# Kernel optimization log

Measured on AMD Instinct MI355X. Metric: run time of the kernel, lower is better.

## Reference

```python
import jax, jax.numpy as jnp
import numpy as np

NUM_ENT = 40000
NUM_REL = 100
EMBED_DIM = 256
FEAT_DIM = 768
BATCH = 32
SEQ_LEN = 3
MASK_POS = 2
EPS = 1e-12


def setup_inputs() -> dict:
    key = jax.random.key(0)
    k1, k2, k3, k4 = jax.random.split(key, 4)
    ent_pkl = jax.random.normal(k1, (NUM_ENT, FEAT_DIM), dtype=jnp.float32)
    other_emb = jax.random.normal(k2, (NUM_ENT + NUM_REL + 3 - NUM_ENT, EMBED_DIM), dtype=jnp.float32)
    proj_W = jax.random.normal(k3, (EMBED_DIM, FEAT_DIM), dtype=jnp.float32) * (1.0 / np.sqrt(FEAT_DIM))
    batch_input_ids = jax.random.randint(k4, (BATCH, SEQ_LEN), 0, NUM_ENT + NUM_REL + 3, dtype=jnp.int64)
    return {
        "ent_pkl": ent_pkl,
        "other_emb": other_emb,
        "proj_W": proj_W,
        "batch_input_ids": batch_input_ids,
        "batch_mask_position": MASK_POS,
    }


def reference(ent_pkl, other_emb, proj_W, batch_input_ids, batch_mask_position):
    # unity embeddings: [other[0], proj(ent_pkl), other[1:]] -> [num_ent+num_rel+3, d]
    ent_proj = ent_pkl @ proj_W.T  # Linear(feat_dim, embed_dim, bias=False)
    unity = jnp.concatenate([other_emb[:1], ent_proj, other_emb[1:]], axis=0)

    mp = int(batch_mask_position)
    # drop the masked slot, keep up to 3 tokens total -> [B, 2]
    query_input = jnp.concatenate(
        [batch_input_ids[:, :mp], batch_input_ids[:, mp + 1:3]], axis=1)
    query_emb = unity[query_input]  # [B, 2, d]
    # F.normalize(dim=-1): x / max(||x||_2, eps)
    norm = jnp.sqrt(jnp.sum(query_emb * query_emb, axis=-1, keepdims=True))
    query_emb = query_emb / jnp.maximum(norm, EPS)
    query_sum = jnp.sum(query_emb, axis=1)  # [B, d]

    E_embed = unity[:NUM_ENT + 1]  # [num_ent+1, d]
    # broadcast L1 distance: [B, num_ent+1]
    score = -jnp.sum(jnp.abs(query_sum[:, None, :] - E_embed[None, :, :]), axis=-1)
    return score
```

## Files before the change

### kernel.cpp

```cpp
#include <hip/hip_runtime.h>
#include <hip/hip_bf16.h>
#include <stdint.h>

#define NE 40000
#define FD 768
#define ED 256
#define NB 32
#define OUTC (NE + 1)

typedef __bf16 bf16x8 __attribute__((ext_vector_type(8)));
typedef float f32x4 __attribute__((ext_vector_type(4)));
typedef unsigned short ushortx8 __attribute__((ext_vector_type(8)));

#define WS_QS 0
#define WS_N01 (32 * 1024)
#define WS_WB (96 * 1024)

__device__ __forceinline__ unsigned short f2bf(float x) {
    union { float f; unsigned u; } v; v.f = x;
    unsigned r = v.u + 0x7fffu + ((v.u >> 16) & 1u);
    return (unsigned short)(r >> 16);
}

__global__ __launch_bounds__(256) void prep_kernel(
    const float* __restrict__ ent_pkl, const float* __restrict__ W,
    const int* __restrict__ ids, const int* __restrict__ mpos,
    unsigned short* __restrict__ Wb, float* __restrict__ n01_raw)
{
    const int bid = blockIdx.x;
    const int t = threadIdx.x;

    if (bid < 192) {
        int i = bid * 1024 + t * 4;
        float4 v = *(const float4*)(W + i);
        ushort4 o;
        o.x = f2bf(v.x); o.y = f2bf(v.y); o.z = f2bf(v.z); o.w = f2bf(v.w);
        *(ushort4*)(Wb + i) = o;
        return;
    }

    __shared__ float row[FD];
    const int slot = bid - 192;
    const int b = slot >> 1, s = slot & 1;
    const int mp = mpos[0];
    const int col = (s < mp) ? s : s + 1;
    const bool wide = (ids[1] == 0 && ids[3] == 0 && ids[5] == 0);
    const int flat = b * 3 + col;
    const int idx = wide ? ids[flat * 2] : ids[flat];
    if (!(idx >= 1 && idx <= NE)) return;

    const float* src = ent_pkl + (size_t)(idx - 1) * FD;
    for (int k = t; k < FD; k += 256) row[k] = src[k];
    __syncthreads();

    const float4* w4 = (const float4*)(W + (size_t)t * FD);
    const float4* r4 = (const float4*)row;
    float a0 = 0.f, a1 = 0.f, a2 = 0.f, a3 = 0.f;
#pragma unroll 2
    for (int k4 = 0; k4 < FD / 4; k4 += 4) {
        float4 w0 = w4[k4 + 0], r0 = r4[k4 + 0];
        float4 w1 = w4[k4 + 1], r1 = r4[k4 + 1];
        float4 w2 = w4[k4 + 2], r2 = r4[k4 + 2];
        float4 w3 = w4[k4 + 3], r3 = r4[k4 + 3];
        a0 += w0.x * r0.x + w0.y * r0.y + w0.z * r0.z + w0.w * r0.w;
        a1 += w1.x * r1.x + w1.y * r1.y + w1.z * r1.z + w1.w * r1.w;
        a2 += w2.x * r2.x + w2.y * r2.y + w2.z * r2.z + w2.w * r2.w;
        a3 += w3.x * r3.x + w3.y * r3.y + w3.z * r3.z + w3.w * r3.w;
    }
    n01_raw[slot * ED + t] = (a0 + a1) + (a2 + a3);
}

__global__ __launch_bounds__(256) void qsum_kernel(
    const float* __restrict__ other_emb, const float* __restrict__ n01_raw,
    const int* __restrict__ ids, const int* __restrict__ mpos,
    float* __restrict__ qs, float* __restrict__ out)
{
    __shared__ float red[4];
    __shared__ float nshare;
    const int b = blockIdx.x, t = threadIdx.x;
    const int mp = mpos[0];
    const bool wide = (ids[1] == 0 && ids[3] == 0 && ids[5] == 0);

    float q = 0.f;
#pragma unroll
    for (int s = 0; s < 2; ++s) {
        const int col = (s < mp) ? s : s + 1;
        const int flat = b * 3 + col;
        const int idx = wide ? ids[flat * 2] : ids[flat];
        float v;
        if (idx >= 1 && idx <= NE) v = n01_raw[(b * 2 + s) * ED + t];
        else if (idx == 0) v = other_emb[t];
        else v = other_emb[(size_t)(idx - NE) * ED + t];

        float ss = v * v;
#pragma unroll
        for (int o = 32; o > 0; o >>= 1) ss += __shfl_down(ss, o, 64);
        if ((t & 63) == 0) red[t >> 6] = ss;
        __syncthreads();
        if (t == 0) nshare = fmaxf(sqrtf(red[0] + red[1] + red[2] + red[3]), 1e-12f);
        __syncthreads();
        q += v / nshare;
        __syncthreads();
    }
    qs[b * ED + t] = q;

    float d = fabsf(q - other_emb[t]);
#pragma unroll
    for (int o = 32; o > 0; o >>= 1) d += __shfl_down(d, o, 64);
    if ((t & 63) == 0) red[t >> 6] = d;
    __syncthreads();
    if (t == 0) out[(size_t)b * OUTC] = -(red[0] + red[1] + red[2] + red[3]);
}

#define APITCH 776
#define SPITCH 132
#define QPITCH 260

__global__ __launch_bounds__(512, 6) void gemm_score_kernel(
    const float* __restrict__ ent_pkl, const unsigned short* __restrict__ Wb,
    const float* __restrict__ qs, float* __restrict__ out)
{
    __shared__ __align__(16) unsigned char smem[50176];
    unsigned short* Asm = (unsigned short*)smem;
    float* Lq = (float*)smem;
    float* S = (float*)(smem + 33280);

    const int t = threadIdx.x;
    const int l = t & 63;
    const int w = t >> 6;
    const int ln15 = l & 15;
    const int lq = l >> 4;
    const int r0 = blockIdx.x * 32;

    {
        const int srow = t >> 4;
        const int seg = (t & 15) * 48;
        const float* ap = ent_pkl + (size_t)(r0 + srow) * FD + seg;
        unsigned short* dst = Asm + srow * APITCH + seg;
#pragma unroll
        for (int j = 0; j < 6; ++j) {
            float4 x = *(const float4*)(ap + j * 8);
            float4 y = *(const float4*)(ap + j * 8 + 4);
            ushortx8 v;
            v[0] = f2bf(x.x); v[1] = f2bf(x.y); v[2] = f2bf(x.z); v[3] = f2bf(x.w);
            v[4] = f2bf(y.x); v[5] = f2bf(y.y); v[6] = f2bf(y.z); v[7] = f2bf(y.w);
            *(ushortx8*)(dst + j * 8) = v;
        }
    }
    __syncthreads();

    f32x4 acc[2][2];
#pragma unroll
    for (int cg = 0; cg < 2; ++cg)
#pragma unroll
        for (int s = 0; s < 2; ++s) acc[cg][s] = (f32x4){0.f, 0.f, 0.f, 0.f};

    const unsigned short* a0p = Asm + ln15 * APITCH + lq * 8;
    const unsigned short* a1p = a0p + 16 * APITCH;
#pragma unroll
    for (int cg = 0; cg < 2; ++cg) {
        const unsigned short* bcol =
            Wb + (size_t)(cg * 128 + w * 16 + ln15) * FD + lq * 8;
#pragma unroll
        for (int h = 0; h < 2; ++h) {
            bf16x8 bfr[12];
#pragma unroll
            for (int c = 0; c < 12; ++c)
                bfr[c] = *(const bf16x8*)(bcol + (h * 12 + c) * 32);
#pragma unroll
            for (int c = 0; c < 12; ++c) {
                const int off = (h * 12 + c) * 32;
                bf16x8 a0 = *(const bf16x8*)(a0p + off);
                bf16x8 a1 = *(const bf16x8*)(a1p + off);
                acc[cg][0] = __builtin_amdgcn_mfma_f32_16x16x32_bf16(a0, bfr[c], acc[cg][0], 0, 0, 0);
                acc[cg][1] = __builtin_amdgcn_mfma_f32_16x16x32_bf16(a1, bfr[c], acc[cg][1], 0, 0, 0);
            }
        }
    }
    __syncthreads();

    {
        const int b = t >> 4;
        const int dseg = (t & 15) * 16;
        const float* src = qs + b * ED + dseg;
        float* dst = Lq + b * QPITCH + dseg;
#pragma unroll
        for (int j = 0; j < 4; ++j)
            *(float4*)(dst + j * 4) = *(const float4*)(src + j * 4);
    }
#pragma unroll
    for (int s = 0; s < 2; ++s)
#pragma unroll
        for (int r = 0; r < 4; ++r)
            S[(s * 16 + lq * 4 + r) * SPITCH + w * 16 + ln15] = acc[0][s][r];
    __syncthreads();

    const int sb = t & 31;
    const int ep = t >> 5;
    float s0 = 0.f, s1 = 0.f;

#pragma unroll
    for (int cg = 0; cg < 2; ++cg) {
        if (cg == 1) {
            __syncthreads();
#pragma unroll
            for (int s = 0; s < 2; ++s)
#pragma unroll
                for (int r = 0; r < 4; ++r)
                    S[(s * 16 + lq * 4 + r) * SPITCH + w * 16 + ln15] = acc[1][s][r];
            __syncthreads();
        }
        const float* q = Lq + sb * QPITCH + cg * 128;
        const float* x0 = S + (2 * ep) * SPITCH;
        const float* x1 = x0 + SPITCH;
#pragma unroll 8
        for (int d = 0; d < 128; d += 4) {
            float4 qv = *(const float4*)(q + d);
            float4 a = *(const float4*)(x0 + d);
            float4 b = *(const float4*)(x1 + d);
            s0 += fabsf(qv.x - a.x) + fabsf(qv.y - a.y) + fabsf(qv.z - a.z) + fabsf(qv.w - a.w);
            s1 += fabsf(qv.x - b.x) + fabsf(qv.y - b.y) + fabsf(qv.z - b.z) + fabsf(qv.w - b.w);
        }
    }
    float* op = out + (size_t)sb * OUTC + 1 + r0 + 2 * ep;
    op[0] = -s0;
    op[1] = -s1;
}

extern "C" void kernel_launch(void* const* d_in, const int* in_sizes, int n_in,
                              void* d_out, int out_size, void* d_ws, size_t ws_size,
                              hipStream_t stream) {
    const float* ent_pkl = (const float*)d_in[0];
    const float* other_emb = (const float*)d_in[1];
    const float* proj_W = (const float*)d_in[2];
    const int* ids = (const int*)d_in[3];
    const int* mpos = (const int*)d_in[4];
    float* out = (float*)d_out;

    float* qs = (float*)((char*)d_ws + WS_QS);
    float* n01_raw = (float*)((char*)d_ws + WS_N01);
    unsigned short* Wb = (unsigned short*)((char*)d_ws + WS_WB);

    prep_kernel<<<256, 256, 0, stream>>>(ent_pkl, proj_W, ids, mpos, Wb, n01_raw);
    qsum_kernel<<<NB, 256, 0, stream>>>(other_emb, n01_raw, ids, mpos, qs, out);
    gemm_score_kernel<<<NE / 32, 512, 0, stream>>>(ent_pkl, Wb, qs, out);
}
```

Before: 274.0 us.

## Restructure GEMM-score kernel with 64-row tiles, 32x32 MFMA and bf16 staging

The fused GEMM and L1-score kernel now handles 64 entity rows per block instead of 32, halving the grid. It uses 32x32x16 bf16 MFMA and loads the A tile in two K-halves into an XOR-swizzled LDS buffer to avoid bank conflicts. The projected embeddings are staged in LDS as bf16, and each lane scores one entity against four queries read directly from global memory. This aims to raise MFMA efficiency, amortise W loads, and reduce LDS traffic in the distance phase. In exchange it adds bf16 rounding of the projected values before the L1 distance and an extra barrier round.

```diff
diff --git a/kernel.cpp b/kernel.cpp
--- a/kernel.cpp
+++ b/kernel.cpp
@@ -10,22 +10,23 @@
 
 typedef __bf16 bf16x8 __attribute__((ext_vector_type(8)));
 typedef float f32x4 __attribute__((ext_vector_type(4)));
-typedef unsigned short ushortx8 __attribute__((ext_vector_type(8)));
+typedef float f32x16 __attribute__((ext_vector_type(16)));
 
 #define WS_QS 0
 #define WS_N01 (32 * 1024)
 #define WS_WB (96 * 1024)
 
-__device__ __forceinline__ unsigned short f2bf(float x) {
-    union { float f; unsigned u; } v; v.f = x;
-    unsigned r = v.u + 0x7fffu + ((v.u >> 16) & 1u);
-    return (unsigned short)(r >> 16);
+__device__ __forceinline__ float bflo(unsigned u) {
+    union { unsigned u; float f; } v; v.u = u << 16; return v.f;
+}
+__device__ __forceinline__ float bfhi(unsigned u) {
+    union { unsigned u; float f; } v; v.u = u & 0xffff0000u; return v.f;
 }
 
 __global__ __launch_bounds__(256) void prep_kernel(
     const float* __restrict__ ent_pkl, const float* __restrict__ W,
     const int* __restrict__ ids, const int* __restrict__ mpos,
-    unsigned short* __restrict__ Wb, float* __restrict__ n01_raw)
+    __bf16* __restrict__ Wb, float* __restrict__ n01_raw)
 {
     const int bid = blockIdx.x;
     const int t = threadIdx.x;
@@ -33,9 +34,8 @@
     if (bid < 192) {
         int i = bid * 1024 + t * 4;
         float4 v = *(const float4*)(W + i);
-        ushort4 o;
-        o.x = f2bf(v.x); o.y = f2bf(v.y); o.z = f2bf(v.z); o.w = f2bf(v.w);
-        *(ushort4*)(Wb + i) = o;
+        __bf16 o[4] = {(__bf16)v.x, (__bf16)v.y, (__bf16)v.z, (__bf16)v.w};
+        *(ushort4*)(Wb + i) = *(const ushort4*)o;
         return;
     }
 
@@ -112,119 +112,99 @@
     if (t == 0) out[(size_t)b * OUTC] = -(red[0] + red[1] + red[2] + red[3]);
 }
 
-#define APITCH 776
-#define SPITCH 132
-#define QPITCH 260
+#define SP 264
 
 __global__ __launch_bounds__(512, 6) void gemm_score_kernel(
-    const float* __restrict__ ent_pkl, const unsigned short* __restrict__ Wb,
+    const float* __restrict__ ent_pkl, const __bf16* __restrict__ Wb,
     const float* __restrict__ qs, float* __restrict__ out)
 {
-    __shared__ __align__(16) unsigned char smem[50176];
-    unsigned short* Asm = (unsigned short*)smem;
-    float* Lq = (float*)smem;
-    float* S = (float*)(smem + 33280);
+    __shared__ __align__(16) unsigned char smem[49152];
+    __bf16* Asm = (__bf16*)smem;
+    __bf16* Sb = (__bf16*)smem;
 
     const int t = threadIdx.x;
     const int l = t & 63;
     const int w = t >> 6;
-    const int ln15 = l & 15;
-    const int lq = l >> 4;
-    const int r0 = blockIdx.x * 32;
-
-    {
-        const int srow = t >> 4;
-        const int seg = (t & 15) * 48;
-        const float* ap = ent_pkl + (size_t)(r0 + srow) * FD + seg;
-        unsigned short* dst = Asm + srow * APITCH + seg;
-#pragma unroll
-        for (int j = 0; j < 6; ++j) {
-            float4 x = *(const float4*)(ap + j * 8);
-            float4 y = *(const float4*)(ap + j * 8 + 4);
-            ushortx8 v;
-            v[0] = f2bf(x.x); v[1] = f2bf(x.y); v[2] = f2bf(x.z); v[3] = f2bf(x.w);
-            v[4] = f2bf(y.x); v[5] = f2bf(y.y); v[6] = f2bf(y.z); v[7] = f2bf(y.w);
-            *(ushortx8*)(dst + j * 8) = v;
-        }
-    }
-    __syncthreads();
-
-    f32x4 acc[2][2];
-#pragma unroll
-    for (int cg = 0; cg < 2; ++cg)
-#pragma unroll
-        for (int s = 0; s < 2; ++s) acc[cg][s] = (f32x4){0.f, 0.f, 0.f, 0.f};
-
-    const unsigned short* a0p = Asm + ln15 * APITCH + lq * 8;
-    const unsigned short* a1p = a0p + 16 * APITCH;
-#pragma unroll
-    for (int cg = 0; cg < 2; ++cg) {
-        const unsigned short* bcol =
-            Wb + (size_t)(cg * 128 + w * 16 + ln15) * FD + lq * 8;
-#pragma unroll
-        for (int h = 0; h < 2; ++h) {
-            bf16x8 bfr[12];
-#pragma unroll
-            for (int c = 0; c < 12; ++c)
-                bfr[c] = *(const bf16x8*)(bcol + (h * 12 + c) * 32);
-#pragma unroll
-            for (int c = 0; c < 12; ++c) {
-                const int off = (h * 12 + c) * 32;
-                bf16x8 a0 = *(const bf16x8*)(a0p + off);
-                bf16x8 a1 = *(const bf16x8*)(a1p + off);
-                acc[cg][0] = __builtin_amdgcn_mfma_f32_16x16x32_bf16(a0, bfr[c], acc[cg][0], 0, 0, 0);
-                acc[cg][1] = __builtin_amdgcn_mfma_f32_16x16x32_bf16(a1, bfr[c], acc[cg][1], 0, 0, 0);
+    const int m31 = l & 31;
+    const int dh = l >> 5;
+    const int e0 = blockIdx.x * 64;
+
+    f32x16 acc0 = {0.f}, acc1 = {0.f};
+#pragma unroll
+    for (int i = 0; i < 16; ++i) { acc0[i] = 0.f; acc1[i] = 0.f; }
+
+    const int srow = t >> 3;
+    const int sseg = t & 7;
+    const int ssw = srow & 7;
+    const __bf16* brow = Wb + (size_t)(32 * w + m31) * FD + dh * 8;
+    const __bf16* arow0 = Asm + m31 * 384;
+    const __bf16* arow1 = Asm + (32 + m31) * 384;
+    const int asw = m31 & 7;
+
+#pragma unroll
+    for (int h = 0; h < 2; ++h) {
+        __syncthreads();
+        {
+            const float* ap = ent_pkl + (size_t)(e0 + srow) * FD + h * 384 + sseg * 48;
+            __bf16* dst = Asm + srow * 384;
+#pragma unroll
+            for (int j = 0; j < 6; ++j) {
+                float4 x = *(const float4*)(ap + j * 8);
+                float4 y = *(const float4*)(ap + j * 8 + 4);
+                bf16x8 v;
+                v[0] = (__bf16)x.x; v[1] = (__bf16)x.y; v[2] = (__bf16)x.z; v[3] = (__bf16)x.w;
+                v[4] = (__bf16)y.x; v[5] = (__bf16)y.y; v[6] = (__bf16)y.z; v[7] = (__bf16)y.w;
+                *(bf16x8*)(dst + ((sseg * 6 + j) ^ ssw) * 8) = v;
             }
         }
-    }
-    __syncthreads();
-
-    {
-        const int b = t >> 4;
-        const int dseg = (t & 15) * 16;
-        const float* src = qs + b * ED + dseg;
-        float* dst = Lq + b * QPITCH + dseg;
-#pragma unroll
-        for (int j = 0; j < 4; ++j)
-            *(float4*)(dst + j * 4) = *(const float4*)(src + j * 4);
-    }
-#pragma unroll
-    for (int s = 0; s < 2; ++s)
-#pragma unroll
-        for (int r = 0; r < 4; ++r)
-            S[(s * 16 + lq * 4 + r) * SPITCH + w * 16 + ln15] = acc[0][s][r];
-    __syncthreads();
-
-    const int sb = t & 31;
-    const int ep = t >> 5;
-    float s0 = 0.f, s1 = 0.f;
-
-#pragma unroll
-    for (int cg = 0; cg < 2; ++cg) {
-        if (cg == 1) {
-            __syncthreads();
-#pragma unroll
-            for (int s = 0; s < 2; ++s)
-#pragma unroll
-                for (int r = 0; r < 4; ++r)
-                    S[(s * 16 + lq * 4 + r) * SPITCH + w * 16 + ln15] = acc[1][s][r];
-            __syncthreads();
+        __syncthreads();
+#pragma unroll 4
+        for (int c = 0; c < 24; ++c) {
+            bf16x8 bv = *(const bf16x8*)(brow + h * 384 + c * 16);
+            const int oct = (2 * c + dh) ^ asw;
+            bf16x8 a0 = *(const bf16x8*)(arow0 + oct * 8);
+            bf16x8 a1 = *(const bf16x8*)(arow1 + oct * 8);
+            acc0 = __builtin_amdgcn_mfma_f32_32x32x16_bf16(a0, bv, acc0, 0, 0, 0);
+            acc1 = __builtin_amdgcn_mfma_f32_32x32x16_bf16(a1, bv, acc1, 0, 0, 0);
         }
-        const float* q = Lq + sb * QPITCH + cg * 128;
-        const float* x0 = S + (2 * ep) * SPITCH;
-        const float* x1 = x0 + SPITCH;
-#pragma unroll 8
-        for (int d = 0; d < 128; d += 4) {
-            float4 qv = *(const float4*)(q + d);
-            float4 a = *(const float4*)(x0 + d);
-            float4 b = *(const float4*)(x1 + d);
-            s0 += fabsf(qv.x - a.x) + fabsf(qv.y - a.y) + fabsf(qv.z - a.z) + fabsf(qv.w - a.w);
-            s1 += fabsf(qv.x - b.x) + fabsf(qv.y - b.y) + fabsf(qv.z - b.z) + fabsf(qv.w - b.w);
-        }
-    }
-    float* op = out + (size_t)sb * OUTC + 1 + r0 + 2 * ep;
-    op[0] = -s0;
-    op[1] = -s1;
+    }
+
+    __syncthreads();
+#pragma unroll
+    for (int r = 0; r < 16; ++r) {
+        const int erow = (r & 3) + 8 * (r >> 2) + 4 * dh;
+        Sb[erow * SP + 32 * w + m31] = (__bf16)acc0[r];
+        Sb[(32 + erow) * SP + 32 * w + m31] = (__bf16)acc1[r];
+    }
+    __syncthreads();
+
+    const int wu = __builtin_amdgcn_readfirstlane(w);
+    const float4* q0 = (const float4*)(qs + (4 * wu + 0) * ED);
+    const float4* q1 = (const float4*)(qs + (4 * wu + 1) * ED);
+    const float4* q2 = (const float4*)(qs + (4 * wu + 2) * ED);
+    const float4* q3 = (const float4*)(qs + (4 * wu + 3) * ED);
+    const unsigned* xrow = (const unsigned*)(Sb + l * SP);
+
+    float s0 = 0.f, s1 = 0.f, s2 = 0.f, s3 = 0.f;
+#pragma unroll 2
+    for (int c = 0; c < 64; ++c) {
+        uint2 xd = *(const uint2*)(xrow + c * 2);
+        float x0 = bflo(xd.x), x1 = bfhi(xd.x);
+        float x2 = bflo(xd.y), x3 = bfhi(xd.y);
+        float4 qa = q0[c];
+        float4 qb = q1[c];
+        float4 qc = q2[c];
+        float4 qd = q3[c];
+        s0 += fabsf(qa.x - x0) + fabsf(qa.y - x1) + fabsf(qa.z - x2) + fabsf(qa.w - x3);
+        s1 += fabsf(qb.x - x0) + fabsf(qb.y - x1) + fabsf(qb.z - x2) + fabsf(qb.w - x3);
+        s2 += fabsf(qc.x - x0) + fabsf(qc.y - x1) + fabsf(qc.z - x2) + fabsf(qc.w - x3);
+        s3 += fabsf(qd.x - x0) + fabsf(qd.y - x1) + fabsf(qd.z - x2) + fabsf(qd.w - x3);
+    }
+    float* ob = out + 1 + e0 + l;
+    ob[(size_t)(4 * wu + 0) * OUTC] = -s0;
+    ob[(size_t)(4 * wu + 1) * OUTC] = -s1;
+    ob[(size_t)(4 * wu + 2) * OUTC] = -s2;
+    ob[(size_t)(4 * wu + 3) * OUTC] = -s3;
 }
 
 extern "C" void kernel_launch(void* const* d_in, const int* in_sizes, int n_in,
@@ -239,9 +219,9 @@
 
     float* qs = (float*)((char*)d_ws + WS_QS);
     float* n01_raw = (float*)((char*)d_ws + WS_N01);
-    unsigned short* Wb = (unsigned short*)((char*)d_ws + WS_WB);
+    __bf16* Wb = (__bf16*)((char*)d_ws + WS_WB);
 
     prep_kernel<<<256, 256, 0, stream>>>(ent_pkl, proj_W, ids, mpos, Wb, n01_raw);
     qsum_kernel<<<NB, 256, 0, stream>>>(other_emb, n01_raw, ids, mpos, qs, out);
-    gemm_score_kernel<<<NE / 32, 512, 0, stream>>>(ent_pkl, Wb, qs, out);
-}
+    gemm_score_kernel<<<NE / 64, 512, 0, stream>>>(ent_pkl, Wb, qs, out);
+}
```

Result: faster. 260.5 us (-4.9%).
